# Performance work log

Hardware: AMD Instinct MI355X
Metric: run time of the kernel (lower is better)

Reference implementation:

```python
import jax, jax.numpy as jnp
import numpy as np

M, N = 1024, 4096


def setup_inputs() -> dict:
    key = jax.random.key(0)
    k1, k2, k3 = jax.random.split(key, 3)
    scores = jax.random.normal(k1, (M, N), dtype=jnp.float32)
    continuing_ag = jax.random.randint(k2, (M,), 0, 2).astype(jnp.int32)
    joint_action_prev = jax.random.randint(k3, (M,), 0, N).astype(jnp.int32)
    return {"scores": scores, "continuing_ag": continuing_ag,
            "joint_action_prev": joint_action_prev}


def _assign(policy, continuing_ag, joint_action_prev):
    """Sequential greedy bipartite assignment (train=False / argmax path)."""
    m, n = policy.shape
    cont = continuing_ag.astype(bool)
    # Pre-assign continuing agents and zero their rows and chosen columns.
    out0 = jnp.where(cont, joint_action_prev, jnp.full((m,), -1, jnp.int32))
    col_hit = (jnp.zeros((n,), jnp.float32)
               .at[joint_action_prev].add(continuing_ag.astype(jnp.float32))) > 0
    pol0 = policy * (~cont)[:, None].astype(policy.dtype) * (~col_hit)[None, :].astype(policy.dtype)
    rows = jnp.arange(m)
    cols = jnp.arange(n)

    def step(carry, i):
        pol, act = carry
        flat = pol.reshape(-1)
        idx = jnp.argmax(flat)
        # skip if this agent is continuing, or all entries already zeroed
        do = (~cont[i]) & jnp.any(flat > 0)
        a = idx // n
        t = (idx % n).astype(act.dtype)
        act = act.at[a].set(jnp.where(do, t, act[a]))
        keep = ~((rows == a)[:, None] | (cols == (idx % n))[None, :])
        pol = jnp.where(do, pol * keep.astype(pol.dtype), pol)
        return (pol, act), None

    (_, act), _ = jax.lax.scan(step, (pol0, out0), jnp.arange(m))
    return act


def reference(scores, continuing_ag, joint_action_prev):
    # get_policy: softmax over the flattened M*N score matrix
    policy = jax.nn.softmax(scores.reshape(-1)).reshape(scores.shape)
    actions = _assign(policy, continuing_ag, joint_action_prev)
    return actions, policy
```

## Files before the change

### kernel.cpp

```cpp
#include <hip/hip_runtime.h>
#include <cstdint>
#include <cstddef>

#define MROWS 1024
#define NCOLS 4096
#define TOPK 8
#define NKEYS (MROWS * TOPK)

typedef unsigned long long u64;
typedef unsigned int u32;

__device__ inline u32 fkey(u32 b) { return (b & 0x80000000u) ? ~b : (b | 0x80000000u); }

__device__ inline int key_col(u64 k) { return (NCOLS - 1) - (int)(k & 0xFFFull); }
__device__ inline int key_row(u64 k) { return (MROWS - 1) - (int)((k >> 12) & 0x3FFull); }

#define WAVE_FENCE() __asm__ volatile("s_waitcnt lgkmcnt(0)" ::: "memory")

__device__ inline float wave_sum_f(float v) {
    #pragma unroll
    for (int off = 32; off >= 1; off >>= 1)
        v += __shfl_xor(v, off, 64);
    return v;
}
__device__ inline u64 wave_max_u64(u64 v) {
    #pragma unroll
    for (int off = 32; off >= 1; off >>= 1) {
        u64 o = __shfl_xor(v, off, 64);
        v = o > v ? o : v;
    }
    return v;
}
__device__ inline u64 umax64(u64 a, u64 b) { return a > b ? a : b; }

__device__ inline u64 wave_max_key(u64 v) {
    u32 h = (u32)(v >> 32);
    u32 hm = h;
    #pragma unroll
    for (int off = 32; off >= 1; off >>= 1) {
        u32 o = __shfl_xor(hm, off, 64);
        hm = o > hm ? o : hm;
    }
    u64 tie = __ballot(h == hm);
    if ((tie & (tie - 1ull)) == 0ull) {
        int src = __ffsll((long long)tie) - 1;
        return __shfl(v, src, 64);
    }
    u32 l = (h == hm) ? (u32)v : 0u;
    #pragma unroll
    for (int off = 32; off >= 1; off >>= 1) {
        u32 o = __shfl_xor(l, off, 64);
        l = o > l ? o : l;
    }
    return ((u64)hm << 32) | l;
}

__global__ __launch_bounds__(256) void k_prep(const float* __restrict__ s,
                                              const int* __restrict__ cont,
                                              const int* __restrict__ prev,
                                              float* __restrict__ rowsum,
                                              unsigned* __restrict__ bitmap_g,
                                              u64* __restrict__ outkeys) {
    __shared__ unsigned lbm[NCOLS / 32];
    __shared__ u64 wavecand[4 * TOPK];
    __shared__ float fred[4];
    int r = blockIdx.x, t = threadIdx.x;
    int wid = t >> 6, lane = t & 63;

    if (t < 128) lbm[t] = 0u;
    __syncthreads();
    for (int i = t; i < MROWS; i += 256) {
        if (cont[i]) {
            int c = prev[i];
            atomicOr(&lbm[c >> 5], 1u << (c & 31));
        }
    }
    __syncthreads();
    if (r == 0 && t < 128) bitmap_g[t] = lbm[t];

    int cg_ = cont[r];
    const float4* s4 = (const float4*)(s + (size_t)r * NCOLS);
    u64 rowpart = (u64)(MROWS - 1 - r) << 12;
    u64 mykeys[16];
    float acc = 0.0f;
    #pragma unroll
    for (int i = 0; i < 4; ++i) {
        int f = t + i * 256;
        float4 v = s4[f];
        acc += expf(v.x) + expf(v.y) + expf(v.z) + expf(v.w);
        int c0 = 4 * f;
        unsigned bmw = lbm[c0 >> 5];
        float se[4] = {v.x, v.y, v.z, v.w};
        #pragma unroll
        for (int e = 0; e < 4; ++e) {
            int c = c0 + e;
            u64 kk = 0ull;
            if (!cg_ && !((bmw >> (c & 31)) & 1u))
                kk = ((u64)fkey(__float_as_uint(se[e])) << 22) | rowpart |
                     (u64)(NCOLS - 1 - c);
            mykeys[i * 4 + e] = kk;
        }
    }
    acc = wave_sum_f(acc);
    if (lane == 0) fred[wid] = acc;
    __syncthreads();
    if (t == 0) rowsum[r] = fred[0] + fred[1] + fred[2] + fred[3];

    u64 tmax = 0ull;
    #pragma unroll
    for (int k = 0; k < 16; ++k) tmax = umax64(tmax, mykeys[k]);
    for (int pass = 0; pass < TOPK; ++pass) {
        u64 w = wave_max_key(tmax);
        if (lane == 0) wavecand[wid * TOPK + pass] = w;
        if (tmax == w && w != 0ull) {
            #pragma unroll
            for (int k = 0; k < 16; ++k)
                if (mykeys[k] == w) mykeys[k] = 0ull;
            tmax = 0ull;
            #pragma unroll
            for (int k = 0; k < 16; ++k) tmax = umax64(tmax, mykeys[k]);
        }
    }
    __syncthreads();
    if (wid == 0) {
        u64 val = (lane < 32) ? wavecand[lane] : 0ull;
        for (int pass = 0; pass < TOPK; ++pass) {
            u64 g = wave_max_key(val);
            if (lane == 0) outkeys[(size_t)r * TOPK + pass] = g;
            if (val == g && g != 0ull) val = 0ull;
        }
    }
}

__global__ __launch_bounds__(1024) void k_policy_match(const float* __restrict__ s,
                                                       const int* __restrict__ cont,
                                                       const int* __restrict__ prev,
                                                       const float* __restrict__ rowsum,
                                                       const unsigned* __restrict__ bitmap,
                                                       const u64* __restrict__ keys_g,
                                                       float* __restrict__ policy,
                                                       float* __restrict__ actions) {
    __shared__ u64 colbest[NCOLS];
    __shared__ unsigned coldone[NCOLS / 32];
    __shared__ unsigned rowdone[MROWS / 32];
    __shared__ float act[MROWS];
    __shared__ float fredf[16];
    __shared__ int exh_flag;

    int t = threadIdx.x;

    if (blockIdx.x != 0) {
        int wid = t >> 6, lane = t & 63;
        float sv = rowsum[t];
        sv = wave_sum_f(sv);
        if (lane == 0) fredf[wid] = sv;
        __syncthreads();
        float g = 0.0f;
        #pragma unroll
        for (int i = 0; i < 16; ++i) g += fredf[i];
        float inv = 1.0f / g;
        int r = blockIdx.x - 1;
        const float4* srow4 = (const float4*)(s + (size_t)r * NCOLS);
        float4* prow4 = (float4*)(policy + (size_t)r * NCOLS);
        float4 v = srow4[t];
        float4 pv;
        pv.x = expf(v.x) * inv;
        pv.y = expf(v.y) * inv;
        pv.z = expf(v.z) * inv;
        pv.w = expf(v.w) * inv;
        prow4[t] = pv;
        return;
    }

    #pragma unroll
    for (int i = 0; i < 4; ++i) colbest[t + i * 1024] = 0ull;
    if (t < 128) coldone[t] = bitmap[t];
    if (t < 32) rowdone[t] = 0u;
    if (t == 0) exh_flag = 0;
    __syncthreads();

    int cgf = cont[t];
    act[t] = cgf ? (float)prev[t] : -1.0f;
    if (cgf) atomicOr(&rowdone[t >> 5], 1u << (t & 31));
    bool active = (cgf == 0);

    u64 myk[TOPK];
    {
        const u64* gk = keys_g + (size_t)t * TOPK;
        #pragma unroll
        for (int k = 0; k < TOPK; ++k) myk[k] = gk[k];
    }
    __syncthreads();

    int anyleft = 1;
    for (int round = 1; round < 1000; ++round) {
        u64 tag = (u64)round << 54;
        bool subm = false;
        u64 mybest = 0ull;
        int mycol = 0;
        if (active) {
            u64 best = 0ull;
            #pragma unroll
            for (int k = 0; k < TOPK; ++k) {
                u64 kk = myk[k];
                if (kk != 0ull) {
                    int c = key_col(kk);
                    if ((coldone[c >> 5] >> (c & 31)) & 1u) { myk[k] = 0ull; kk = 0ull; }
                }
                best = umax64(best, kk);
            }
            if (best == 0ull) {
                active = false;
                exh_flag = 1;
            } else {
                subm = true;
                mybest = best;
                mycol = key_col(best);
                #pragma unroll
                for (int k = 0; k < TOPK; ++k) {
                    u64 kk = myk[k];
                    if (kk != 0ull) atomicMax(&colbest[key_col(kk)], tag | kk);
                }
            }
        }
        anyleft = __syncthreads_count(active ? 1 : 0);
        if (anyleft == 0) break;
        if (subm && colbest[mycol] == (tag | mybest)) {
            act[t] = (float)mycol;
            atomicOr(&coldone[mycol >> 5], 1u << (mycol & 31));
            atomicOr(&rowdone[t >> 5], 1u << (t & 31));
            active = false;
        }
        __syncthreads();
    }
    __syncthreads();

    if ((exh_flag || anyleft) && t < 64) {
        int lane0 = t;
        for (int guard = 0; guard < 1200; ++guard) {
            u64 best = 0ull;
            for (int rr = 0; rr < MROWS; ++rr) {
                if ((rowdone[rr >> 5] >> (rr & 31)) & 1u) continue;
                const float* srow = s + (size_t)rr * NCOLS;
                u64 rp = (u64)(MROWS - 1 - rr) << 12;
                for (int c = lane0; c < NCOLS; c += 64) {
                    if ((coldone[c >> 5] >> (c & 31)) & 1u) continue;
                    u64 kk = ((u64)fkey(__float_as_uint(srow[c])) << 22) | rp |
                             (u64)(NCOLS - 1 - c);
                    best = umax64(best, kk);
                }
            }
            best = wave_max_u64(best);
            if (best == 0ull) break;
            if (lane0 == 0) {
                int row = key_row(best), col = key_col(best);
                rowdone[row >> 5] |= 1u << (row & 31);
                coldone[col >> 5] |= 1u << (col & 31);
                act[row] = (float)col;
            }
            WAVE_FENCE();
        }
    }
    __syncthreads();
    actions[t] = act[t];
}

extern "C" void kernel_launch(void* const* d_in, const int* in_sizes, int n_in,
                              void* d_out, int out_size, void* d_ws, size_t ws_size,
                              hipStream_t stream) {
    (void)in_sizes; (void)n_in; (void)out_size; (void)ws_size;
    const float* scores = (const float*)d_in[0];
    const int* cont = (const int*)d_in[1];
    const int* prev = (const int*)d_in[2];
    float* out = (float*)d_out;
    float* actions = out;
    float* policy = out + MROWS;

    char* ws = (char*)d_ws;
    float* rowsum = (float*)(ws + 0);
    unsigned* bitmap = (unsigned*)(ws + 4096);
    u64* keys8 = (u64*)(ws + 8192);

    k_prep<<<MROWS, 256, 0, stream>>>(scores, cont, prev, rowsum, bitmap, keys8);
    k_policy_match<<<MROWS + 1, 1024, 0, stream>>>(scores, cont, prev, rowsum,
                                                   bitmap, keys8, policy, actions);
}
```

Baseline: 95.34 us.

## Run greedy matching in a single wavefront and shrink policy blocks to 256 threads

The matching block now runs its parallel auction rounds inside one 64-lane wavefront. Each lane handles 16 rows and keeps candidate liveness in bitmasks, and it reads keys from global memory on demand. This replaces the block-wide __syncthreads_count barriers with wave-level fences and ballots. The policy blocks drop to 256 threads that each write four float4 values, and both kernels use the fast __expf. In k_prep the row loads are hoisted ahead of the bitmap setup so their latency overlaps it. The trade-off is more serial work per lane in each round and slightly lower exp precision.

```diff
diff --git a/kernel.cpp b/kernel.cpp
--- a/kernel.cpp
+++ b/kernel.cpp
@@ -5,7 +5,6 @@
 #define MROWS 1024
 #define NCOLS 4096
 #define TOPK 8
-#define NKEYS (MROWS * TOPK)
 
 typedef unsigned long long u64;
 typedef unsigned int u32;
@@ -67,6 +66,13 @@
     int r = blockIdx.x, t = threadIdx.x;
     int wid = t >> 6, lane = t & 63;
 
+    const float4* s4 = (const float4*)(s + (size_t)r * NCOLS);
+    float4 vv[4];
+    vv[0] = s4[t];
+    vv[1] = s4[t + 256];
+    vv[2] = s4[t + 512];
+    vv[3] = s4[t + 768];
+
     if (t < 128) lbm[t] = 0u;
     __syncthreads();
     for (int i = t; i < MROWS; i += 256) {
@@ -79,15 +85,14 @@
     if (r == 0 && t < 128) bitmap_g[t] = lbm[t];
 
     int cg_ = cont[r];
-    const float4* s4 = (const float4*)(s + (size_t)r * NCOLS);
     u64 rowpart = (u64)(MROWS - 1 - r) << 12;
     u64 mykeys[16];
     float acc = 0.0f;
     #pragma unroll
     for (int i = 0; i < 4; ++i) {
+        float4 v = vv[i];
+        acc += __expf(v.x) + __expf(v.y) + __expf(v.z) + __expf(v.w);
         int f = t + i * 256;
-        float4 v = s4[f];
-        acc += expf(v.x) + expf(v.y) + expf(v.z) + expf(v.w);
         int c0 = 4 * f;
         unsigned bmw = lbm[c0 >> 5];
         float se[4] = {v.x, v.y, v.z, v.w};
@@ -132,118 +137,133 @@
     }
 }
 
-__global__ __launch_bounds__(1024) void k_policy_match(const float* __restrict__ s,
-                                                       const int* __restrict__ cont,
-                                                       const int* __restrict__ prev,
-                                                       const float* __restrict__ rowsum,
-                                                       const unsigned* __restrict__ bitmap,
-                                                       const u64* __restrict__ keys_g,
-                                                       float* __restrict__ policy,
-                                                       float* __restrict__ actions) {
+__global__ __launch_bounds__(256) void k_policy_match(const float* __restrict__ s,
+                                                      const int* __restrict__ cont,
+                                                      const int* __restrict__ prev,
+                                                      const float* __restrict__ rowsum,
+                                                      const unsigned* __restrict__ bitmap,
+                                                      const u64* __restrict__ keys_g,
+                                                      float* __restrict__ policy,
+                                                      float* __restrict__ actions) {
     __shared__ u64 colbest[NCOLS];
     __shared__ unsigned coldone[NCOLS / 32];
     __shared__ unsigned rowdone[MROWS / 32];
     __shared__ float act[MROWS];
-    __shared__ float fredf[16];
-    __shared__ int exh_flag;
+    __shared__ float fredf[4];
 
     int t = threadIdx.x;
 
     if (blockIdx.x != 0) {
+        int r = blockIdx.x - 1;
+        const float4* srow4 = (const float4*)(s + (size_t)r * NCOLS);
+        float4 w0 = srow4[t], w1 = srow4[t + 256], w2 = srow4[t + 512], w3 = srow4[t + 768];
+        float sv = rowsum[t] + rowsum[t + 256] + rowsum[t + 512] + rowsum[t + 768];
+        sv = wave_sum_f(sv);
         int wid = t >> 6, lane = t & 63;
-        float sv = rowsum[t];
-        sv = wave_sum_f(sv);
         if (lane == 0) fredf[wid] = sv;
         __syncthreads();
-        float g = 0.0f;
+        float inv = 1.0f / (fredf[0] + fredf[1] + fredf[2] + fredf[3]);
+        float4* prow4 = (float4*)(policy + (size_t)r * NCOLS);
+        float4 p;
+        p.x = __expf(w0.x) * inv; p.y = __expf(w0.y) * inv;
+        p.z = __expf(w0.z) * inv; p.w = __expf(w0.w) * inv;
+        prow4[t] = p;
+        p.x = __expf(w1.x) * inv; p.y = __expf(w1.y) * inv;
+        p.z = __expf(w1.z) * inv; p.w = __expf(w1.w) * inv;
+        prow4[t + 256] = p;
+        p.x = __expf(w2.x) * inv; p.y = __expf(w2.y) * inv;
+        p.z = __expf(w2.z) * inv; p.w = __expf(w2.w) * inv;
+        prow4[t + 512] = p;
+        p.x = __expf(w3.x) * inv; p.y = __expf(w3.y) * inv;
+        p.z = __expf(w3.z) * inv; p.w = __expf(w3.w) * inv;
+        prow4[t + 768] = p;
+        return;
+    }
+
+    if (t >= 64) return;
+    int lane = t;
+
+    #pragma unroll
+    for (int i = 0; i < NCOLS / 64; ++i) colbest[lane + i * 64] = 0ull;
+    coldone[lane] = bitmap[lane];
+    coldone[lane + 64] = bitmap[lane + 64];
+    if (lane < 32) rowdone[lane] = 0u;
+    WAVE_FENCE();
+
+    u32 rowact = 0u;
+    u64 kal0 = 0ull, kal1 = 0ull;
+    #pragma unroll
+    for (int j = 0; j < 16; ++j) {
+        int r = lane * 16 + j;
+        int cg = cont[r];
+        act[r] = cg ? (float)prev[r] : -1.0f;
+        if (cg) {
+            atomicOr(&rowdone[r >> 5], 1u << (r & 31));
+        } else {
+            rowact |= (1u << j);
+            if (j < 8) kal0 |= (0xFFull << (8 * j));
+            else       kal1 |= (0xFFull << (8 * (j - 8)));
+        }
+    }
+    WAVE_FENCE();
+
+    bool exh_l = false;
+    const u64* gk = keys_g + (size_t)lane * (16 * TOPK);
+    u64 bestv[16];
+    #pragma unroll
+    for (int j = 0; j < 16; ++j) bestv[j] = 0ull;
+
+    for (int round = 1; round < 1100; ++round) {
+        u64 tag = (u64)round << 54;
         #pragma unroll
-        for (int i = 0; i < 16; ++i) g += fredf[i];
-        float inv = 1.0f / g;
-        int r = blockIdx.x - 1;
-        const float4* srow4 = (const float4*)(s + (size_t)r * NCOLS);
-        float4* prow4 = (float4*)(policy + (size_t)r * NCOLS);
-        float4 v = srow4[t];
-        float4 pv;
-        pv.x = expf(v.x) * inv;
-        pv.y = expf(v.y) * inv;
-        pv.z = expf(v.z) * inv;
-        pv.w = expf(v.w) * inv;
-        prow4[t] = pv;
-        return;
-    }
-
-    #pragma unroll
-    for (int i = 0; i < 4; ++i) colbest[t + i * 1024] = 0ull;
-    if (t < 128) coldone[t] = bitmap[t];
-    if (t < 32) rowdone[t] = 0u;
-    if (t == 0) exh_flag = 0;
-    __syncthreads();
-
-    int cgf = cont[t];
-    act[t] = cgf ? (float)prev[t] : -1.0f;
-    if (cgf) atomicOr(&rowdone[t >> 5], 1u << (t & 31));
-    bool active = (cgf == 0);
-
-    u64 myk[TOPK];
-    {
-        const u64* gk = keys_g + (size_t)t * TOPK;
-        #pragma unroll
-        for (int k = 0; k < TOPK; ++k) myk[k] = gk[k];
-    }
-    __syncthreads();
-
-    int anyleft = 1;
-    for (int round = 1; round < 1000; ++round) {
-        u64 tag = (u64)round << 54;
-        bool subm = false;
-        u64 mybest = 0ull;
-        int mycol = 0;
-        if (active) {
+        for (int j = 0; j < 16; ++j) {
+            if (!(rowact & (1u << j))) continue;
+            u32 al = (u32)(((j < 8 ? kal0 : kal1) >> (8 * (j & 7))) & 0xFFull);
+            u32 nal = al;
             u64 best = 0ull;
             #pragma unroll
             for (int k = 0; k < TOPK; ++k) {
-                u64 kk = myk[k];
-                if (kk != 0ull) {
-                    int c = key_col(kk);
-                    if ((coldone[c >> 5] >> (c & 31)) & 1u) { myk[k] = 0ull; kk = 0ull; }
-                }
+                if (!(al & (1u << k))) continue;
+                u64 kk = gk[j * TOPK + k];
+                if (kk == 0ull) { nal &= ~(1u << k); continue; }
+                int c = key_col(kk);
+                if ((coldone[c >> 5] >> (c & 31)) & 1u) { nal &= ~(1u << k); continue; }
+                atomicMax((u64*)&colbest[c], tag | kk);
                 best = umax64(best, kk);
             }
-            if (best == 0ull) {
-                active = false;
-                exh_flag = 1;
-            } else {
-                subm = true;
-                mybest = best;
-                mycol = key_col(best);
-                #pragma unroll
-                for (int k = 0; k < TOPK; ++k) {
-                    u64 kk = myk[k];
-                    if (kk != 0ull) atomicMax(&colbest[key_col(kk)], tag | kk);
-                }
+            if (j < 8) kal0 = (kal0 & ~(0xFFull << (8 * j))) | ((u64)nal << (8 * j));
+            else       kal1 = (kal1 & ~(0xFFull << (8 * (j - 8)))) | ((u64)nal << (8 * (j - 8)));
+            if (nal == 0u) { rowact &= ~(1u << j); exh_l = true; bestv[j] = 0ull; }
+            else bestv[j] = best;
+        }
+        WAVE_FENCE();
+        #pragma unroll
+        for (int j = 0; j < 16; ++j) {
+            if (!(rowact & (1u << j)) || bestv[j] == 0ull) continue;
+            int c = key_col(bestv[j]);
+            if (colbest[c] == (tag | bestv[j])) {
+                int r = lane * 16 + j;
+                act[r] = (float)c;
+                atomicOr(&coldone[c >> 5], 1u << (c & 31));
+                atomicOr(&rowdone[r >> 5], 1u << (r & 31));
+                rowact &= ~(1u << j);
             }
         }
-        anyleft = __syncthreads_count(active ? 1 : 0);
-        if (anyleft == 0) break;
-        if (subm && colbest[mycol] == (tag | mybest)) {
-            act[t] = (float)mycol;
-            atomicOr(&coldone[mycol >> 5], 1u << (mycol & 31));
-            atomicOr(&rowdone[t >> 5], 1u << (t & 31));
-            active = false;
-        }
-        __syncthreads();
-    }
-    __syncthreads();
-
-    if ((exh_flag || anyleft) && t < 64) {
-        int lane0 = t;
+        WAVE_FENCE();
+        if (__ballot(rowact != 0u) == 0ull) break;
+    }
+    bool leftover = (__ballot((int)(rowact != 0u)) != 0ull);
+    bool doFB = leftover || (__ballot((int)exh_l) != 0ull);
+    WAVE_FENCE();
+
+    if (doFB) {
         for (int guard = 0; guard < 1200; ++guard) {
             u64 best = 0ull;
             for (int rr = 0; rr < MROWS; ++rr) {
                 if ((rowdone[rr >> 5] >> (rr & 31)) & 1u) continue;
                 const float* srow = s + (size_t)rr * NCOLS;
                 u64 rp = (u64)(MROWS - 1 - rr) << 12;
-                for (int c = lane0; c < NCOLS; c += 64) {
+                for (int c = lane; c < NCOLS; c += 64) {
                     if ((coldone[c >> 5] >> (c & 31)) & 1u) continue;
                     u64 kk = ((u64)fkey(__float_as_uint(srow[c])) << 22) | rp |
                              (u64)(NCOLS - 1 - c);
@@ -252,7 +272,7 @@
             }
             best = wave_max_u64(best);
             if (best == 0ull) break;
-            if (lane0 == 0) {
+            if (lane == 0) {
                 int row = key_row(best), col = key_col(best);
                 rowdone[row >> 5] |= 1u << (row & 31);
                 coldone[col >> 5] |= 1u << (col & 31);
@@ -261,8 +281,8 @@
             WAVE_FENCE();
         }
     }
-    __syncthreads();
-    actions[t] = act[t];
+    WAVE_FENCE();
+    for (int i = lane; i < MROWS; i += 64) actions[i] = act[i];
 }
 
 extern "C" void kernel_launch(void* const* d_in, const int* in_sizes, int n_in,
@@ -282,6 +302,6 @@
     u64* keys8 = (u64*)(ws + 8192);
 
     k_prep<<<MROWS, 256, 0, stream>>>(scores, cont, prev, rowsum, bitmap, keys8);
-    k_policy_match<<<MROWS + 1, 1024, 0, stream>>>(scores, cont, prev, rowsum,
-                                                   bitmap, keys8, policy, actions);
-}
+    k_policy_match<<<MROWS + 1, 256, 0, stream>>>(scores, cont, prev, rowsum,
+                                                  bitmap, keys8, policy, actions);
+}
```

After: 150.4 us. 1.58x slower.

## Move continuing-agent masking into matcher and add candidate-list tail phase

Applied to the files above, without the earlier changes.

The prep kernel no longer builds the continuing-column bitmap or masks keys per row. Masking of continuing columns now happens in the matcher's shared-memory init. The auction loop now exits once 96 or fewer rows remain active. Those rows' surviving top-K candidates are gathered into a shared list and resolved greedily by one wave, with a full scan of the scores matrix kept only as a last fallback. The expf calls become __expf and per-candidate atomics are fused into the filtering loop. The aim is to cut redundant per-block bitmap work and the many late synchronised rounds. The cost is less exact exp and a risk of a slow fallback scan if the list misses rows.

```diff
diff --git a/kernel.cpp b/kernel.cpp
--- a/kernel.cpp
+++ b/kernel.cpp
@@ -5,7 +5,6 @@
 #define MROWS 1024
 #define NCOLS 4096
 #define TOPK 8
-#define NKEYS (MROWS * TOPK)
 
 typedef unsigned long long u64;
 typedef unsigned int u32;
@@ -56,29 +55,13 @@
 }
 
 __global__ __launch_bounds__(256) void k_prep(const float* __restrict__ s,
-                                              const int* __restrict__ cont,
-                                              const int* __restrict__ prev,
                                               float* __restrict__ rowsum,
-                                              unsigned* __restrict__ bitmap_g,
                                               u64* __restrict__ outkeys) {
-    __shared__ unsigned lbm[NCOLS / 32];
     __shared__ u64 wavecand[4 * TOPK];
     __shared__ float fred[4];
     int r = blockIdx.x, t = threadIdx.x;
     int wid = t >> 6, lane = t & 63;
 
-    if (t < 128) lbm[t] = 0u;
-    __syncthreads();
-    for (int i = t; i < MROWS; i += 256) {
-        if (cont[i]) {
-            int c = prev[i];
-            atomicOr(&lbm[c >> 5], 1u << (c & 31));
-        }
-    }
-    __syncthreads();
-    if (r == 0 && t < 128) bitmap_g[t] = lbm[t];
-
-    int cg_ = cont[r];
     const float4* s4 = (const float4*)(s + (size_t)r * NCOLS);
     u64 rowpart = (u64)(MROWS - 1 - r) << 12;
     u64 mykeys[16];
@@ -87,18 +70,14 @@
     for (int i = 0; i < 4; ++i) {
         int f = t + i * 256;
         float4 v = s4[f];
-        acc += expf(v.x) + expf(v.y) + expf(v.z) + expf(v.w);
+        acc += __expf(v.x) + __expf(v.y) + __expf(v.z) + __expf(v.w);
         int c0 = 4 * f;
-        unsigned bmw = lbm[c0 >> 5];
         float se[4] = {v.x, v.y, v.z, v.w};
         #pragma unroll
         for (int e = 0; e < 4; ++e) {
             int c = c0 + e;
-            u64 kk = 0ull;
-            if (!cg_ && !((bmw >> (c & 31)) & 1u))
-                kk = ((u64)fkey(__float_as_uint(se[e])) << 22) | rowpart |
-                     (u64)(NCOLS - 1 - c);
-            mykeys[i * 4 + e] = kk;
+            mykeys[i * 4 + e] = ((u64)fkey(__float_as_uint(se[e])) << 22) | rowpart |
+                                (u64)(NCOLS - 1 - c);
         }
     }
     acc = wave_sum_f(acc);
@@ -136,20 +115,23 @@
                                                        const int* __restrict__ cont,
                                                        const int* __restrict__ prev,
                                                        const float* __restrict__ rowsum,
-                                                       const unsigned* __restrict__ bitmap,
                                                        const u64* __restrict__ keys_g,
                                                        float* __restrict__ policy,
                                                        float* __restrict__ actions) {
     __shared__ u64 colbest[NCOLS];
+    __shared__ u64 list[1024];
     __shared__ unsigned coldone[NCOLS / 32];
     __shared__ unsigned rowdone[MROWS / 32];
     __shared__ float act[MROWS];
     __shared__ float fredf[16];
-    __shared__ int exh_flag;
+    __shared__ int cnt;
 
     int t = threadIdx.x;
 
     if (blockIdx.x != 0) {
+        int r = blockIdx.x - 1;
+        const float4* srow4 = (const float4*)(s + (size_t)r * NCOLS);
+        float4 v = srow4[t];
         int wid = t >> 6, lane = t & 63;
         float sv = rowsum[t];
         sv = wave_sum_f(sv);
@@ -159,29 +141,30 @@
         #pragma unroll
         for (int i = 0; i < 16; ++i) g += fredf[i];
         float inv = 1.0f / g;
-        int r = blockIdx.x - 1;
-        const float4* srow4 = (const float4*)(s + (size_t)r * NCOLS);
         float4* prow4 = (float4*)(policy + (size_t)r * NCOLS);
-        float4 v = srow4[t];
         float4 pv;
-        pv.x = expf(v.x) * inv;
-        pv.y = expf(v.y) * inv;
-        pv.z = expf(v.z) * inv;
-        pv.w = expf(v.w) * inv;
+        pv.x = __expf(v.x) * inv;
+        pv.y = __expf(v.y) * inv;
+        pv.z = __expf(v.z) * inv;
+        pv.w = __expf(v.w) * inv;
         prow4[t] = pv;
         return;
     }
 
     #pragma unroll
     for (int i = 0; i < 4; ++i) colbest[t + i * 1024] = 0ull;
-    if (t < 128) coldone[t] = bitmap[t];
+    if (t < 128) coldone[t] = 0u;
     if (t < 32) rowdone[t] = 0u;
-    if (t == 0) exh_flag = 0;
+    if (t == 0) cnt = 0;
     __syncthreads();
 
     int cgf = cont[t];
-    act[t] = cgf ? (float)prev[t] : -1.0f;
-    if (cgf) atomicOr(&rowdone[t >> 5], 1u << (t & 31));
+    int pv_ = prev[t];
+    act[t] = cgf ? (float)pv_ : -1.0f;
+    if (cgf) {
+        atomicOr(&rowdone[t >> 5], 1u << (t & 31));
+        atomicOr(&coldone[pv_ >> 5], 1u << (pv_ & 31));
+    }
     bool active = (cgf == 0);
 
     u64 myk[TOPK];
@@ -193,7 +176,7 @@
     __syncthreads();
 
     int anyleft = 1;
-    for (int round = 1; round < 1000; ++round) {
+    for (int round = 1; round < 400; ++round) {
         u64 tag = (u64)round << 54;
         bool subm = false;
         u64 mybest = 0ull;
@@ -207,20 +190,17 @@
                     int c = key_col(kk);
                     if ((coldone[c >> 5] >> (c & 31)) & 1u) { myk[k] = 0ull; kk = 0ull; }
                 }
-                best = umax64(best, kk);
+                if (kk != 0ull) {
+                    atomicMax((u64*)&colbest[key_col(kk)], tag | kk);
+                    best = umax64(best, kk);
+                }
             }
             if (best == 0ull) {
                 active = false;
-                exh_flag = 1;
             } else {
                 subm = true;
                 mybest = best;
                 mycol = key_col(best);
-                #pragma unroll
-                for (int k = 0; k < TOPK; ++k) {
-                    u64 kk = myk[k];
-                    if (kk != 0ull) atomicMax(&colbest[key_col(kk)], tag | kk);
-                }
             }
         }
         anyleft = __syncthreads_count(active ? 1 : 0);
@@ -232,33 +212,82 @@
             active = false;
         }
         __syncthreads();
-    }
-    __syncthreads();
-
-    if ((exh_flag || anyleft) && t < 64) {
-        int lane0 = t;
-        for (int guard = 0; guard < 1200; ++guard) {
-            u64 best = 0ull;
-            for (int rr = 0; rr < MROWS; ++rr) {
-                if ((rowdone[rr >> 5] >> (rr & 31)) & 1u) continue;
-                const float* srow = s + (size_t)rr * NCOLS;
-                u64 rp = (u64)(MROWS - 1 - rr) << 12;
-                for (int c = lane0; c < NCOLS; c += 64) {
-                    if ((coldone[c >> 5] >> (c & 31)) & 1u) continue;
-                    u64 kk = ((u64)fkey(__float_as_uint(srow[c])) << 22) | rp |
-                             (u64)(NCOLS - 1 - c);
+        if (anyleft <= 96) break;
+    }
+
+    if (anyleft > 0) {
+        if (active) {
+            u64 tmp[TOPK];
+            int nal = 0;
+            #pragma unroll
+            for (int k = 0; k < TOPK; ++k) {
+                u64 kk = myk[k];
+                if (kk == 0ull) continue;
+                int c = key_col(kk);
+                if ((coldone[c >> 5] >> (c & 31)) & 1u) continue;
+                tmp[nal++] = kk;
+            }
+            if (nal) {
+                int base = atomicAdd(&cnt, nal);
+                if (base + nal <= 1024)
+                    for (int i = 0; i < nal; ++i) list[base + i] = tmp[i];
+            }
+        }
+        __syncthreads();
+        if (t < 64) {
+            int lane = t;
+            int n = cnt; if (n > 1024) n = 1024;
+            for (int iter = 0; iter < 200; ++iter) {
+                u64 best = 0ull;
+                for (int i = lane; i < n; i += 64) {
+                    u64 kk = list[i];
+                    if (kk == 0ull) continue;
+                    int c = key_col(kk), rr = key_row(kk);
+                    if (((coldone[c >> 5] >> (c & 31)) & 1u) ||
+                        ((rowdone[rr >> 5] >> (rr & 31)) & 1u)) { list[i] = 0ull; continue; }
                     best = umax64(best, kk);
                 }
-            }
-            best = wave_max_u64(best);
-            if (best == 0ull) break;
-            if (lane0 == 0) {
-                int row = key_row(best), col = key_col(best);
-                rowdone[row >> 5] |= 1u << (row & 31);
-                coldone[col >> 5] |= 1u << (col & 31);
-                act[row] = (float)col;
-            }
-            WAVE_FENCE();
+                best = wave_max_key(best);
+                if (best == 0ull) break;
+                if (lane == 0) {
+                    int rr = key_row(best), c = key_col(best);
+                    act[rr] = (float)c;
+                    coldone[c >> 5] |= 1u << (c & 31);
+                    rowdone[rr >> 5] |= 1u << (rr & 31);
+                }
+                WAVE_FENCE();
+            }
+        }
+    }
+    __syncthreads();
+
+    if (t < 64) {
+        int lane = t;
+        unsigned miss = (lane < 32) ? ~rowdone[lane] : 0u;
+        if (__ballot(miss != 0u) != 0ull) {
+            for (int guard = 0; guard < 1200; ++guard) {
+                u64 best = 0ull;
+                for (int rr = 0; rr < MROWS; ++rr) {
+                    if ((rowdone[rr >> 5] >> (rr & 31)) & 1u) continue;
+                    const float* srow = s + (size_t)rr * NCOLS;
+                    u64 rp = (u64)(MROWS - 1 - rr) << 12;
+                    for (int c = lane; c < NCOLS; c += 64) {
+                        if ((coldone[c >> 5] >> (c & 31)) & 1u) continue;
+                        u64 kk = ((u64)fkey(__float_as_uint(srow[c])) << 22) | rp |
+                                 (u64)(NCOLS - 1 - c);
+                        best = umax64(best, kk);
+                    }
+                }
+                best = wave_max_u64(best);
+                if (best == 0ull) break;
+                if (lane == 0) {
+                    int row = key_row(best), col = key_col(best);
+                    rowdone[row >> 5] |= 1u << (row & 31);
+                    coldone[col >> 5] |= 1u << (col & 31);
+                    act[row] = (float)col;
+                }
+                WAVE_FENCE();
+            }
         }
     }
     __syncthreads();
@@ -278,10 +307,9 @@
 
     char* ws = (char*)d_ws;
     float* rowsum = (float*)(ws + 0);
-    unsigned* bitmap = (unsigned*)(ws + 4096);
     u64* keys8 = (u64*)(ws + 8192);
 
-    k_prep<<<MROWS, 256, 0, stream>>>(scores, cont, prev, rowsum, bitmap, keys8);
+    k_prep<<<MROWS, 256, 0, stream>>>(scores, rowsum, keys8);
     k_policy_match<<<MROWS + 1, 1024, 0, stream>>>(scores, cont, prev, rowsum,
-                                                   bitmap, keys8, policy, actions);
-}
+                                                   keys8, policy, actions);
+}
```

Measured after the change: 206.6 us. 2.17x slower.

## Replace per-row exact top-8 selection with threshold-filtered candidate lists

Applied to the files above, without the earlier changes.

The prep kernel no longer runs repeated wave-max passes to extract an exact top-8 per row. Instead it collects up to 32 score keys above fixed thresholds (2.5 to 4.2, retried when the list overflows) through a shared atomic counter, and stores them column-major for coalesced loads. Continuing-agent row and column masking moves into the matching kernel, and expf becomes __expf. The thresholds assume roughly standard-normal scores. Rows with few candidates depend on the slow serial fallback scan, and the match loop now processes 32 keys per thread, which adds atomics and register pressure.

```diff
diff --git a/kernel.cpp b/kernel.cpp
--- a/kernel.cpp
+++ b/kernel.cpp
@@ -4,8 +4,7 @@
 
 #define MROWS 1024
 #define NCOLS 4096
-#define TOPK 8
-#define NKEYS (MROWS * TOPK)
+#define KCAP 32
 
 typedef unsigned long long u64;
 typedef unsigned int u32;
@@ -33,232 +32,184 @@
 }
 __device__ inline u64 umax64(u64 a, u64 b) { return a > b ? a : b; }
 
-__device__ inline u64 wave_max_key(u64 v) {
-    u32 h = (u32)(v >> 32);
-    u32 hm = h;
-    #pragma unroll
-    for (int off = 32; off >= 1; off >>= 1) {
-        u32 o = __shfl_xor(hm, off, 64);
-        hm = o > hm ? o : hm;
-    }
-    u64 tie = __ballot(h == hm);
-    if ((tie & (tie - 1ull)) == 0ull) {
-        int src = __ffsll((long long)tie) - 1;
-        return __shfl(v, src, 64);
-    }
-    u32 l = (h == hm) ? (u32)v : 0u;
-    #pragma unroll
-    for (int off = 32; off >= 1; off >>= 1) {
-        u32 o = __shfl_xor(l, off, 64);
-        l = o > l ? o : l;
-    }
-    return ((u64)hm << 32) | l;
-}
-
 __global__ __launch_bounds__(256) void k_prep(const float* __restrict__ s,
-                                              const int* __restrict__ cont,
-                                              const int* __restrict__ prev,
                                               float* __restrict__ rowsum,
-                                              unsigned* __restrict__ bitmap_g,
-                                              u64* __restrict__ outkeys) {
-    __shared__ unsigned lbm[NCOLS / 32];
-    __shared__ u64 wavecand[4 * TOPK];
+                                              u64* __restrict__ keys_g) {
     __shared__ float fred[4];
+    __shared__ u64 list[KCAP];
+    __shared__ u32 cnt;
     int r = blockIdx.x, t = threadIdx.x;
-    int wid = t >> 6, lane = t & 63;
-
-    if (t < 128) lbm[t] = 0u;
-    __syncthreads();
-    for (int i = t; i < MROWS; i += 256) {
-        if (cont[i]) {
-            int c = prev[i];
-            atomicOr(&lbm[c >> 5], 1u << (c & 31));
-        }
-    }
-    __syncthreads();
-    if (r == 0 && t < 128) bitmap_g[t] = lbm[t];
-
-    int cg_ = cont[r];
+
     const float4* s4 = (const float4*)(s + (size_t)r * NCOLS);
+    float4 v0 = s4[t], v1 = s4[t + 256], v2 = s4[t + 512], v3 = s4[t + 768];
+    if (t == 0) cnt = 0;
+
+    float se[16] = {v0.x, v0.y, v0.z, v0.w, v1.x, v1.y, v1.z, v1.w,
+                    v2.x, v2.y, v2.z, v2.w, v3.x, v3.y, v3.z, v3.w};
+    float acc = 0.0f;
+    #pragma unroll
+    for (int i = 0; i < 16; ++i) acc += __expf(se[i]);
+    acc = wave_sum_f(acc);
+    if ((t & 63) == 0) fred[t >> 6] = acc;
+
     u64 rowpart = (u64)(MROWS - 1 - r) << 12;
-    u64 mykeys[16];
-    float acc = 0.0f;
-    #pragma unroll
-    for (int i = 0; i < 4; ++i) {
-        int f = t + i * 256;
-        float4 v = s4[f];
-        acc += expf(v.x) + expf(v.y) + expf(v.z) + expf(v.w);
-        int c0 = 4 * f;
-        unsigned bmw = lbm[c0 >> 5];
-        float se[4] = {v.x, v.y, v.z, v.w};
+    __syncthreads();
+
+    for (int attempt = 0; attempt < 4; ++attempt) {
+        float T = attempt == 0 ? 2.5f : attempt == 1 ? 2.9f
+                : attempt == 2 ? 3.4f : 4.2f;
         #pragma unroll
-        for (int e = 0; e < 4; ++e) {
-            int c = c0 + e;
-            u64 kk = 0ull;
-            if (!cg_ && !((bmw >> (c & 31)) & 1u))
-                kk = ((u64)fkey(__float_as_uint(se[e])) << 22) | rowpart |
-                     (u64)(NCOLS - 1 - c);
-            mykeys[i * 4 + e] = kk;
-        }
-    }
-    acc = wave_sum_f(acc);
-    if (lane == 0) fred[wid] = acc;
-    __syncthreads();
+        for (int i = 0; i < 16; ++i) {
+            if (se[i] > T) {
+                u32 slot = atomicAdd(&cnt, 1u);
+                if (slot < KCAP) {
+                    int c = 4 * (t + (i >> 2) * 256) + (i & 3);
+                    list[slot] = ((u64)fkey(__float_as_uint(se[i])) << 22) | rowpart |
+                                 (u64)(NCOLS - 1 - c);
+                }
+            }
+        }
+        __syncthreads();
+        if (cnt <= KCAP) break;
+        __syncthreads();
+        if (t == 0) cnt = 0;
+        __syncthreads();
+    }
+    u32 n = cnt;
+    if (n > KCAP) n = 0;
+    if (t < KCAP)
+        keys_g[(size_t)t * MROWS + r] = (t < n) ? list[t] : 0ull;
     if (t == 0) rowsum[r] = fred[0] + fred[1] + fred[2] + fred[3];
-
-    u64 tmax = 0ull;
-    #pragma unroll
-    for (int k = 0; k < 16; ++k) tmax = umax64(tmax, mykeys[k]);
-    for (int pass = 0; pass < TOPK; ++pass) {
-        u64 w = wave_max_key(tmax);
-        if (lane == 0) wavecand[wid * TOPK + pass] = w;
-        if (tmax == w && w != 0ull) {
-            #pragma unroll
-            for (int k = 0; k < 16; ++k)
-                if (mykeys[k] == w) mykeys[k] = 0ull;
-            tmax = 0ull;
-            #pragma unroll
-            for (int k = 0; k < 16; ++k) tmax = umax64(tmax, mykeys[k]);
-        }
-    }
-    __syncthreads();
-    if (wid == 0) {
-        u64 val = (lane < 32) ? wavecand[lane] : 0ull;
-        for (int pass = 0; pass < TOPK; ++pass) {
-            u64 g = wave_max_key(val);
-            if (lane == 0) outkeys[(size_t)r * TOPK + pass] = g;
-            if (val == g && g != 0ull) val = 0ull;
-        }
-    }
-}
-
-__global__ __launch_bounds__(1024) void k_policy_match(const float* __restrict__ s,
-                                                       const int* __restrict__ cont,
-                                                       const int* __restrict__ prev,
-                                                       const float* __restrict__ rowsum,
-                                                       const unsigned* __restrict__ bitmap,
-                                                       const u64* __restrict__ keys_g,
-                                                       float* __restrict__ policy,
-                                                       float* __restrict__ actions) {
+}
+
+__global__ __launch_bounds__(1024, 1) void k_policy_match(const float* __restrict__ s,
+                                                          const int* __restrict__ cont,
+                                                          const int* __restrict__ prev,
+                                                          const float* __restrict__ rowsum,
+                                                          const u64* __restrict__ keys_g,
+                                                          float* __restrict__ policy,
+                                                          float* __restrict__ actions) {
     __shared__ u64 colbest[NCOLS];
-    __shared__ unsigned coldone[NCOLS / 32];
-    __shared__ unsigned rowdone[MROWS / 32];
+    __shared__ u32 coldone[NCOLS / 32];
+    __shared__ u32 rowdone[MROWS / 32];
     __shared__ float act[MROWS];
     __shared__ float fredf[16];
-    __shared__ int exh_flag;
 
     int t = threadIdx.x;
 
     if (blockIdx.x != 0) {
-        int wid = t >> 6, lane = t & 63;
+        int r = blockIdx.x - 1;
+        const float4* srow4 = (const float4*)(s + (size_t)r * NCOLS);
+        float4 v = srow4[t];
         float sv = rowsum[t];
         sv = wave_sum_f(sv);
-        if (lane == 0) fredf[wid] = sv;
+        if ((t & 63) == 0) fredf[t >> 6] = sv;
         __syncthreads();
         float g = 0.0f;
         #pragma unroll
         for (int i = 0; i < 16; ++i) g += fredf[i];
         float inv = 1.0f / g;
-        int r = blockIdx.x - 1;
-        const float4* srow4 = (const float4*)(s + (size_t)r * NCOLS);
         float4* prow4 = (float4*)(policy + (size_t)r * NCOLS);
-        float4 v = srow4[t];
-        float4 pv;
-        pv.x = expf(v.x) * inv;
-        pv.y = expf(v.y) * inv;
-        pv.z = expf(v.z) * inv;
-        pv.w = expf(v.w) * inv;
-        prow4[t] = pv;
+        float4 p;
+        p.x = __expf(v.x) * inv;
+        p.y = __expf(v.y) * inv;
+        p.z = __expf(v.z) * inv;
+        p.w = __expf(v.w) * inv;
+        prow4[t] = p;
         return;
     }
 
     #pragma unroll
     for (int i = 0; i < 4; ++i) colbest[t + i * 1024] = 0ull;
-    if (t < 128) coldone[t] = bitmap[t];
+    if (t < 128) coldone[t] = 0u;
     if (t < 32) rowdone[t] = 0u;
-    if (t == 0) exh_flag = 0;
     __syncthreads();
 
     int cgf = cont[t];
-    act[t] = cgf ? (float)prev[t] : -1.0f;
-    if (cgf) atomicOr(&rowdone[t >> 5], 1u << (t & 31));
+    int pv_ = prev[t];
+    act[t] = cgf ? (float)pv_ : -1.0f;
+    if (cgf) {
+        atomicOr(&rowdone[t >> 5], 1u << (t & 31));
+        atomicOr(&coldone[pv_ >> 5], 1u << (pv_ & 31));
+    }
     bool active = (cgf == 0);
 
-    u64 myk[TOPK];
-    {
-        const u64* gk = keys_g + (size_t)t * TOPK;
-        #pragma unroll
-        for (int k = 0; k < TOPK; ++k) myk[k] = gk[k];
-    }
-    __syncthreads();
-
-    int anyleft = 1;
-    for (int round = 1; round < 1000; ++round) {
+    u64 kk[KCAP];
+    #pragma unroll
+    for (int k = 0; k < KCAP; ++k) kk[k] = keys_g[(size_t)k * MROWS + t];
+    __syncthreads();
+
+    for (int round = 1; round < 400; ++round) {
         u64 tag = (u64)round << 54;
-        bool subm = false;
-        u64 mybest = 0ull;
-        int mycol = 0;
+        bool sub = false;
+        u64 best = 0ull;
         if (active) {
-            u64 best = 0ull;
             #pragma unroll
-            for (int k = 0; k < TOPK; ++k) {
-                u64 kk = myk[k];
-                if (kk != 0ull) {
-                    int c = key_col(kk);
-                    if ((coldone[c >> 5] >> (c & 31)) & 1u) { myk[k] = 0ull; kk = 0ull; }
-                }
-                best = umax64(best, kk);
+            for (int h = 0; h < 2; ++h) {
+                u32 cw[16];
+                #pragma unroll
+                for (int k = 0; k < 16; ++k) {
+                    int c = key_col(kk[h * 16 + k]);
+                    cw[k] = coldone[c >> 5];
+                }
+                #pragma unroll
+                for (int k = 0; k < 16; ++k) {
+                    int c = key_col(kk[h * 16 + k]);
+                    if ((cw[k] >> (c & 31)) & 1u) kk[h * 16 + k] = 0ull;
+                    best = umax64(best, kk[h * 16 + k]);
+                }
             }
             if (best == 0ull) {
                 active = false;
-                exh_flag = 1;
             } else {
-                subm = true;
-                mybest = best;
-                mycol = key_col(best);
+                sub = true;
                 #pragma unroll
-                for (int k = 0; k < TOPK; ++k) {
-                    u64 kk = myk[k];
-                    if (kk != 0ull) atomicMax(&colbest[key_col(kk)], tag | kk);
-                }
-            }
-        }
-        anyleft = __syncthreads_count(active ? 1 : 0);
-        if (anyleft == 0) break;
-        if (subm && colbest[mycol] == (tag | mybest)) {
-            act[t] = (float)mycol;
-            atomicOr(&coldone[mycol >> 5], 1u << (mycol & 31));
-            atomicOr(&rowdone[t >> 5], 1u << (t & 31));
-            active = false;
-        }
-        __syncthreads();
-    }
-    __syncthreads();
-
-    if ((exh_flag || anyleft) && t < 64) {
-        int lane0 = t;
-        for (int guard = 0; guard < 1200; ++guard) {
-            u64 best = 0ull;
-            for (int rr = 0; rr < MROWS; ++rr) {
-                if ((rowdone[rr >> 5] >> (rr & 31)) & 1u) continue;
-                const float* srow = s + (size_t)rr * NCOLS;
-                u64 rp = (u64)(MROWS - 1 - rr) << 12;
-                for (int c = lane0; c < NCOLS; c += 64) {
-                    if ((coldone[c >> 5] >> (c & 31)) & 1u) continue;
-                    u64 kk = ((u64)fkey(__float_as_uint(srow[c])) << 22) | rp |
-                             (u64)(NCOLS - 1 - c);
-                    best = umax64(best, kk);
-                }
-            }
-            best = wave_max_u64(best);
-            if (best == 0ull) break;
-            if (lane0 == 0) {
-                int row = key_row(best), col = key_col(best);
-                rowdone[row >> 5] |= 1u << (row & 31);
-                coldone[col >> 5] |= 1u << (col & 31);
-                act[row] = (float)col;
-            }
-            WAVE_FENCE();
+                for (int k = 0; k < KCAP; ++k)
+                    if (kk[k] != 0ull)
+                        atomicMax((u64*)&colbest[key_col(kk[k])], tag | kk[k]);
+            }
+        }
+        __syncthreads();
+        if (sub && colbest[key_col(best)] == (tag | best)) {
+            int c = key_col(best);
+            u32 old = atomicOr(&coldone[c >> 5], 1u << (c & 31));
+            if (!(old & (1u << (c & 31)))) {
+                act[t] = (float)c;
+                atomicOr(&rowdone[t >> 5], 1u << (t & 31));
+                active = false;
+            }
+        }
+        int left = __syncthreads_count(active ? 1 : 0);
+        if (left == 0) break;
+    }
+    __syncthreads();
+
+    if (t < 64) {
+        u32 miss = (t < 32) ? ~rowdone[t] : 0u;
+        if (__ballot(miss != 0u) != 0ull) {
+            for (int guard = 0; guard < 1200; ++guard) {
+                u64 best = 0ull;
+                for (int rr = 0; rr < MROWS; ++rr) {
+                    if ((rowdone[rr >> 5] >> (rr & 31)) & 1u) continue;
+                    const float* srow = s + (size_t)rr * NCOLS;
+                    u64 rp = (u64)(MROWS - 1 - rr) << 12;
+                    for (int c = t; c < NCOLS; c += 64) {
+                        if ((coldone[c >> 5] >> (c & 31)) & 1u) continue;
+                        u64 kk2 = ((u64)fkey(__float_as_uint(srow[c])) << 22) | rp |
+                                  (u64)(NCOLS - 1 - c);
+                        best = umax64(best, kk2);
+                    }
+                }
+                best = wave_max_u64(best);
+                if (best == 0ull) break;
+                if (t == 0) {
+                    int row = key_row(best), col = key_col(best);
+                    rowdone[row >> 5] |= 1u << (row & 31);
+                    coldone[col >> 5] |= 1u << (col & 31);
+                    act[row] = (float)col;
+                }
+                WAVE_FENCE();
+            }
         }
     }
     __syncthreads();
@@ -278,10 +229,9 @@
 
     char* ws = (char*)d_ws;
     float* rowsum = (float*)(ws + 0);
-    unsigned* bitmap = (unsigned*)(ws + 4096);
-    u64* keys8 = (u64*)(ws + 8192);
-
-    k_prep<<<MROWS, 256, 0, stream>>>(scores, cont, prev, rowsum, bitmap, keys8);
+    u64* keys32 = (u64*)(ws + 8192);
+
+    k_prep<<<MROWS, 256, 0, stream>>>(scores, rowsum, keys32);
     k_policy_match<<<MROWS + 1, 1024, 0, stream>>>(scores, cont, prev, rowsum,
-                                                   bitmap, keys8, policy, actions);
-}
+                                                   keys32, policy, actions);
+}
```

New measurement: 91.69 us. 3.8% less time.
